# Performance work log

Measured on AMD Instinct MI355X. Metric: run time of the kernel, lower is better.

Reference implementation:

```python
import jax, jax.numpy as jnp
import numpy as np

B, S, D, H = 4, 2048, 1024, 16
HD = D // H  # head_dim = 64


def setup_inputs() -> dict:
    key = jax.random.key(0)
    ks = jax.random.split(key, 5)
    scale = 1.0 / np.sqrt(D)  # xavier-ish
    return {
        "query": jax.random.normal(ks[0], (B, S, D), dtype=jnp.float32),
        "Wq": jax.random.normal(ks[1], (D, D), dtype=jnp.float32) * scale,
        "bq": jnp.zeros((D,), dtype=jnp.float32),
        "Wk": jax.random.normal(ks[2], (D, D), dtype=jnp.float32) * scale,
        "bk": jnp.zeros((D,), dtype=jnp.float32),
        "Wv": jax.random.normal(ks[3], (D, D), dtype=jnp.float32) * scale,
        "bv": jnp.zeros((D,), dtype=jnp.float32),
        "Wo": jax.random.normal(ks[4], (D, D), dtype=jnp.float32) * scale,
        "bo": jnp.zeros((D,), dtype=jnp.float32),
    }


def reference(query, Wq, bq, Wk, bk, Wv, bv, Wo, bo):
    # Self-attention: key = value = query. Linear layers use y = x @ W^T + b (torch nn.Linear).
    q = query @ Wq.T + bq
    k = query @ Wk.T + bk
    v = query @ Wv.T + bv
    # [B, S, D] -> [B, H, S, HD]
    q = q.reshape(B, S, H, HD).transpose(0, 2, 1, 3)
    k = k.reshape(B, S, H, HD).transpose(0, 2, 1, 3)
    v = v.reshape(B, S, H, HD).transpose(0, 2, 1, 3)
    scores = jnp.einsum('bhqd,bhkd->bhqk', q, k) / jnp.sqrt(jnp.float32(HD))
    attn = jax.nn.softmax(scores, axis=-1)  # dropout=0 (eval)
    out = jnp.einsum('bhqk,bhkd->bhqd', attn, v)
    out = out.transpose(0, 2, 1, 3).reshape(B, S, D)
    out = out @ Wo.T + bo
    return out
```

## Files before the change

kernel.cpp:

```cpp
#include <hip/hip_runtime.h>
#include <cstdint>


#define B_ 4
#define S_ 2048
#define D_ 1024
#define H_ 16
#define HD_ 64
#define QKV_N 3072
#define QK_LD 2048
#define SCALE_Q 0.18033688011111772f

typedef __bf16 bf16x8 __attribute__((ext_vector_type(8)));
typedef __bf16 bf16x2 __attribute__((ext_vector_type(2)));
typedef float f32x4 __attribute__((ext_vector_type(4)));
typedef short short8 __attribute__((ext_vector_type(8)));

__device__ __forceinline__ unsigned short f2bf(float f) {
  unsigned int u = __builtin_bit_cast(unsigned int, f);
  u = (u + 0x7FFFu + ((u >> 16) & 1u)) >> 16;
  return (unsigned short)u;
}

__device__ __forceinline__ unsigned int pkbf(float a, float b) {
  bf16x2 v;
  v.x = (__bf16)a;
  v.y = (__bf16)b;
  return __builtin_bit_cast(unsigned int, v);
}

__device__ __forceinline__ void gload16(const void* g, void* l) {
  __builtin_amdgcn_global_load_lds(
      (const __attribute__((address_space(1))) void*)g,
      (__attribute__((address_space(3))) void*)l, 16, 0, 0);
}

__global__ __launch_bounds__(256) void cvt_bf16(const float* __restrict__ in,
                                                unsigned short* __restrict__ out, int n8) {
  int i = blockIdx.x * 256 + threadIdx.x;
  if (i >= n8) return;
  const float4* p = (const float4*)in + (size_t)i * 2;
  float4 a = p[0], b = p[1];
  unsigned short o[8] = {f2bf(a.x), f2bf(a.y), f2bf(a.z), f2bf(a.w),
                         f2bf(b.x), f2bf(b.y), f2bf(b.z), f2bf(b.w)};
  *(uint4*)(out + (size_t)i * 8) = *(const uint4*)o;
}

__global__ __launch_bounds__(256) void cvt_w4(const float* __restrict__ w0, const float* __restrict__ w1,
                                              const float* __restrict__ w2, const float* __restrict__ w3,
                                              unsigned short* __restrict__ dst) {
  int y = blockIdx.y;
  const float* src = (y == 0) ? w0 : (y == 1) ? w1 : (y == 2) ? w2 : w3;
  float s = (y == 0) ? SCALE_Q : 1.0f;
  int i = blockIdx.x * 256 + threadIdx.x;
  const float4* p = (const float4*)src + (size_t)i * 2;
  float4 a = p[0], b = p[1];
  unsigned short o[8] = {f2bf(a.x * s), f2bf(a.y * s), f2bf(a.z * s), f2bf(a.w * s),
                         f2bf(b.x * s), f2bf(b.y * s), f2bf(b.z * s), f2bf(b.w * s)};
  *(uint4*)(dst + (size_t)y * 1048576 + (size_t)i * 8) = *(const uint4*)o;
}

__global__ __launch_bounds__(256) void bias_cat(const float* __restrict__ bq, const float* __restrict__ bk,
                                                const float* __restrict__ bv, float* __restrict__ bcat) {
  int i = blockIdx.x * 256 + threadIdx.x;
  float v = (i < 1024) ? bq[i] * SCALE_Q : (i < 2048) ? bk[i - 1024] : bv[i - 2048];
  bcat[i] = v;
}

__device__ __forceinline__ void ld_afrag(const unsigned short* s, int rowbase, int quad,
                                         int sw, bf16x8 af[4][2]) {
#pragma unroll
  for (int mi2 = 0; mi2 < 4; ++mi2) {
    int row = rowbase + mi2 * 16;
#pragma unroll
    for (int kk = 0; kk < 2; ++kk)
      af[mi2][kk] = *(const bf16x8*)&s[row * 64 + ((((kk << 2) + quad) ^ sw) << 3)];
  }
}

__device__ __forceinline__ void ld_bfrag(const unsigned short* s, int rowbase, int quad,
                                         int sw, bf16x8 bf[2][2]) {
#pragma unroll
  for (int ni2 = 0; ni2 < 2; ++ni2) {
    int row = rowbase + ni2 * 16;
#pragma unroll
    for (int kk = 0; kk < 2; ++kk)
      bf[ni2][kk] = *(const bf16x8*)&s[row * 64 + ((((kk << 2) + quad) ^ sw) << 3)];
  }
}

#define SBAR() __builtin_amdgcn_sched_barrier(0)
#define BARRIER()                      \
  do {                                 \
    SBAR();                            \
    __builtin_amdgcn_s_barrier();      \
    SBAR();                            \
  } while (0)
#define WAITLGKM()                                      \
  do {                                                  \
    asm volatile("s_waitcnt lgkmcnt(0)" ::: "memory");  \
    SBAR();                                             \
  } while (0)

#define MM(qm, qn, BF)                                                                   \
  _Pragma("unroll") for (int mi2 = 0; mi2 < 4; ++mi2)                                    \
  _Pragma("unroll") for (int ni2 = 0; ni2 < 2; ++ni2)                                    \
  _Pragma("unroll") for (int kk = 0; kk < 2; ++kk)                                       \
      acc[(qm) * 4 + mi2][(qn) * 2 + ni2] = __builtin_amdgcn_mfma_f32_16x16x32_bf16(     \
          af[mi2][kk], BF[ni2][kk], acc[(qm) * 4 + mi2][(qn) * 2 + ni2], 0, 0, 0);

__global__ __launch_bounds__(512, 2) void gemm_qkv_256(
    const unsigned short* __restrict__ A, const unsigned short* __restrict__ W,
    const float* __restrict__ bias, unsigned short* __restrict__ qk,
    unsigned short* __restrict__ vt) {
  __shared__ __attribute__((aligned(16))) unsigned short sA[2][256 * 64];
  __shared__ __attribute__((aligned(16))) unsigned short sB[2][256 * 64];

  const int t = threadIdx.x;
  const int lane = t & 63;
  const int w = t >> 6;
  const int lm = lane & 15;
  const int quad = lane >> 4;
  const int sw = lm & 7;
  const int wm = (w >> 2) * 128;
  const int wn = (w & 3) * 64;

  const int bid = blockIdx.x;
  const int xcd = bid & 7, lin = bid >> 3;
  const int mt = xcd * 4 + (lin & 3);
  const int nt = lin >> 2;
  const int m0 = mt * 256, n0 = nt * 256;
  const int K = 1024;

  const int srow = t >> 3;
  const int scol = ((t & 7) ^ ((t >> 3) & 7)) << 3;
  const unsigned short* Ab = A + ((size_t)m0 + srow) * K + scol;
  const unsigned short* Wb = W + ((size_t)n0 + srow) * K + scol;

#define STG_A(bb, q, kt) gload16(Ab + (size_t)((q) * 64) * K + (kt), &sA[bb][(q) * 4096 + w * 512])
#define STG_B(bb, q, kt) gload16(Wb + (size_t)((q) * 64) * K + (kt), &sB[bb][(q) * 4096 + w * 512])

  STG_A(0, 0, 0); STG_A(0, 1, 0); STG_A(0, 2, 0); STG_A(0, 3, 0);
  STG_B(0, 0, 0); STG_B(0, 1, 0); STG_B(0, 2, 0); STG_B(0, 3, 0);
  STG_A(1, 0, 64); STG_A(1, 2, 64);
  STG_B(1, 0, 64); STG_B(1, 1, 64);
  STG_A(1, 1, 64); STG_A(1, 3, 64);
  asm volatile("s_waitcnt vmcnt(6)" ::: "memory");
  BARRIER();

  f32x4 acc[8][4] = {};
  bf16x8 af[4][2], bf0[2][2], bf1[2][2];

#define GROUP(c, kn1, kn2)                                                            \
  do {                                                                                \
    ld_afrag(sA[c], wm + lm, quad, sw, af);                                           \
    ld_bfrag(sB[c], wn + lm, quad, sw, bf0);                                          \
    STG_B(c ^ 1, 2, kn1);                                                             \
    STG_B(c ^ 1, 3, kn1);                                                             \
    BARRIER(); WAITLGKM();                                                            \
    __builtin_amdgcn_s_setprio(1); MM(0, 0, bf0); __builtin_amdgcn_s_setprio(0);      \
    BARRIER();                                                                        \
    ld_bfrag(sB[c], wn + 32 + lm, quad, sw, bf1);                                     \
    STG_A(c, 0, kn2);                                                                 \
    STG_A(c, 2, kn2);                                                                 \
    BARRIER(); WAITLGKM();                                                            \
    __builtin_amdgcn_s_setprio(1); MM(0, 1, bf1); __builtin_amdgcn_s_setprio(0);      \
    BARRIER();                                                                        \
    ld_afrag(sA[c], wm + 64 + lm, quad, sw, af);                                      \
    STG_B(c, 0, kn2);                                                                 \
    STG_B(c, 1, kn2);                                                                 \
    BARRIER(); WAITLGKM();                                                            \
    __builtin_amdgcn_s_setprio(1); MM(1, 0, bf0); __builtin_amdgcn_s_setprio(0);      \
    BARRIER();                                                                        \
    STG_A(c, 1, kn2);                                                                 \
    STG_A(c, 3, kn2);                                                                 \
    asm volatile("s_waitcnt vmcnt(6)" ::: "memory");                                  \
    BARRIER();                                                                        \
    __builtin_amdgcn_s_setprio(1); MM(1, 1, bf1); __builtin_amdgcn_s_setprio(0);      \
    BARRIER();                                                                        \
  } while (0)

  for (int kt = 0; kt < K; kt += 128) {
    const int kn1a = kt + 64;
    const int kn2a = (kt + 128 < K) ? kt + 128 : K - 64;
    const int kn1b = kn2a;
    const int kn2b = (kt + 192 < K) ? kt + 192 : K - 64;
    GROUP(0, kn1a, kn2a);
    GROUP(1, kn1b, kn2b);
  }

  asm volatile("s_waitcnt vmcnt(0)" ::: "memory");

#pragma unroll
  for (int mi = 0; mi < 8; ++mi) {
    const int rbase = m0 + wm + mi * 16 + quad * 4;
#pragma unroll
    for (int ni = 0; ni < 4; ++ni) {
      const int col = n0 + wn + ni * 16 + lm;
      const float bv = bias[col];
      float v0 = acc[mi][ni][0] + bv, v1 = acc[mi][ni][1] + bv;
      float v2 = acc[mi][ni][2] + bv, v3 = acc[mi][ni][3] + bv;
      if (n0 < 2048) {
        qk[(size_t)(rbase + 0) * QK_LD + col] = f2bf(v0);
        qk[(size_t)(rbase + 1) * QK_LD + col] = f2bf(v1);
        qk[(size_t)(rbase + 2) * QK_LD + col] = f2bf(v2);
        qk[(size_t)(rbase + 3) * QK_LD + col] = f2bf(v3);
      } else {
        int c = col - 2048;
        int bh = (m0 >> 11) * 16 + (c >> 6);
        int hd = c & 63;
        int sbase = rbase & 2047;
        uint2 pk = {pkbf(v0, v1), pkbf(v2, v3)};
        *(uint2*)(vt + (size_t)bh * (HD_ * S_) + (size_t)hd * S_ + sbase) = pk;
      }
    }
  }
}

__global__ __launch_bounds__(256) void gemm_bt(
    const unsigned short* __restrict__ A, const unsigned short* __restrict__ W,
    const float* __restrict__ bias, void* __restrict__ Cout,
    unsigned short* __restrict__ vt, int M, int N, int K, int mode) {
  __shared__ __attribute__((aligned(16))) unsigned short sA[128 * 32];
  __shared__ __attribute__((aligned(16))) unsigned short sB[128 * 32];
  const int t = threadIdx.x;
  const int lane = t & 63;
  const int w = t >> 6;
  const int lm = lane & 15;
  const int quad = lane >> 4;
  const int m0 = blockIdx.x * 128;
  const int n0 = blockIdx.y * 128;
  const int wm = (w & 1) * 64;
  const int wn = (w >> 1) * 64;

  const int off0 = t * 8, off1 = t * 8 + 2048;
  const int ar0 = off0 >> 5, ac0 = (((off0 >> 3) & 3) ^ ((ar0 >> 1) & 3)) * 8;
  const int ar1 = off1 >> 5, ac1 = (((off1 >> 3) & 3) ^ ((ar1 >> 1) & 3)) * 8;
  const unsigned short* Ag0 = A + (size_t)(m0 + ar0) * K + ac0;
  const unsigned short* Ag1 = A + (size_t)(m0 + ar1) * K + ac1;
  const unsigned short* Wg0 = W + (size_t)(n0 + ar0) * K + ac0;
  const unsigned short* Wg1 = W + (size_t)(n0 + ar1) * K + ac1;
  unsigned short* sA0 = &sA[w * 512];
  unsigned short* sA1 = &sA[2048 + w * 512];
  unsigned short* sB0 = &sB[w * 512];
  unsigned short* sB1 = &sB[2048 + w * 512];

  f32x4 acc[4][4] = {};

  for (int kt = 0; kt < K; kt += 32) {
    gload16(Ag0 + kt, sA0);
    gload16(Ag1 + kt, sA1);
    gload16(Wg0 + kt, sB0);
    gload16(Wg1 + kt, sB1);
    __syncthreads();
    bf16x8 af[4], bf[4];
#pragma unroll
    for (int mi = 0; mi < 4; ++mi) {
      int row = wm + mi * 16 + lm;
      af[mi] = *(const bf16x8*)&sA[row * 32 + ((quad ^ ((row >> 1) & 3)) << 3)];
    }
#pragma unroll
    for (int ni = 0; ni < 4; ++ni) {
      int row = wn + ni * 16 + lm;
      bf[ni] = *(const bf16x8*)&sB[row * 32 + ((quad ^ ((row >> 1) & 3)) << 3)];
    }
#pragma unroll
    for (int mi = 0; mi < 4; ++mi)
#pragma unroll
      for (int ni = 0; ni < 4; ++ni)
        acc[mi][ni] = __builtin_amdgcn_mfma_f32_16x16x32_bf16(af[mi], bf[ni], acc[mi][ni], 0, 0, 0);
    __syncthreads();
  }

#pragma unroll
  for (int mi = 0; mi < 4; ++mi)
#pragma unroll
    for (int ni = 0; ni < 4; ++ni) {
      int col = n0 + wn + ni * 16 + lm;
      float bv = bias[col];
      float v0 = acc[mi][ni][0] + bv, v1 = acc[mi][ni][1] + bv;
      float v2 = acc[mi][ni][2] + bv, v3 = acc[mi][ni][3] + bv;
      int rbase = m0 + wm + mi * 16 + quad * 4;
      if (mode == 0) {
        float* op = (float*)Cout;
        op[(size_t)(rbase + 0) * N + col] = v0;
        op[(size_t)(rbase + 1) * N + col] = v1;
        op[(size_t)(rbase + 2) * N + col] = v2;
        op[(size_t)(rbase + 3) * N + col] = v3;
      } else if (col < 2048) {
        unsigned short* op = (unsigned short*)Cout;
        op[(size_t)(rbase + 0) * QK_LD + col] = f2bf(v0);
        op[(size_t)(rbase + 1) * QK_LD + col] = f2bf(v1);
        op[(size_t)(rbase + 2) * QK_LD + col] = f2bf(v2);
        op[(size_t)(rbase + 3) * QK_LD + col] = f2bf(v3);
      } else {
        int c = col - 2048;
        int bh = (m0 >> 11) * 16 + (c >> 6);
        int hd = c & 63;
        int sbase = (rbase & 2047);
        uint2 pk = {pkbf(v0, v1), pkbf(v2, v3)};
        *(uint2*)(vt + (size_t)bh * (HD_ * S_) + (size_t)hd * S_ + sbase) = pk;
      }
    }
}

__global__ __launch_bounds__(512, 4) void attn_kernel(
    const unsigned short* __restrict__ qk, const unsigned short* __restrict__ vt,
    unsigned short* __restrict__ ab) {
  __shared__ __attribute__((aligned(16))) unsigned short sK[2][64 * 64];
  __shared__ __attribute__((aligned(16))) unsigned short sV[2][64 * 64];
  __shared__ __attribute__((aligned(16))) unsigned short sP[8][32 * 64];

  const int t = threadIdx.x;
  const int lane = t & 63;
  const int w = t >> 6;
  const int lm = lane & 15;
  const int quad = lane >> 4;
  const int bh = blockIdx.x & 63;
  const int b = bh >> 4, h = bh & 15;
  const int q0 = (blockIdx.x >> 6) * 256;

  const unsigned short* qg = qk + (size_t)b * S_ * QK_LD + h * HD_;
  const unsigned short* kg = qg + 1024;
  const unsigned short* vg = vt + (size_t)bh * HD_ * S_;

  const int r0 = t >> 3;
  const int c0 = ((t & 7) ^ (r0 & 7)) * 8;

  gload16(kg + (size_t)r0 * QK_LD + c0, &sK[0][w * 512]);
  gload16(vg + (size_t)r0 * S_ + c0, &sV[0][w * 512]);

  bf16x8 qf[2][2];
#pragma unroll
  for (int mi = 0; mi < 2; ++mi) {
    int row = q0 + w * 32 + mi * 16 + lm;
#pragma unroll
    for (int kc = 0; kc < 2; ++kc)
      qf[mi][kc] = *(const bf16x8*)(qg + (size_t)row * QK_LD + kc * 32 + quad * 8);
  }
  __syncthreads();

  unsigned short* sPw = sP[w];
  const bf16x8 ones = __builtin_bit_cast(bf16x8, (short8)(short)0x3F80);
  f32x4 o[2][4] = {};
  f32x4 Lacc[2] = {};

  for (int n0 = 0; n0 < S_; n0 += 64) {
    const int cur = (n0 >> 6) & 1, nxt = cur ^ 1;
    if (n0 + 64 < S_) {
      gload16(kg + (size_t)(n0 + 64 + r0) * QK_LD + c0, &sK[nxt][w * 512]);
      gload16(vg + (size_t)r0 * S_ + (n0 + 64) + c0, &sV[nxt][w * 512]);
    }

    f32x4 s[2][4] = {};
#pragma unroll
    for (int kc = 0; kc < 2; ++kc)
#pragma unroll
      for (int nb = 0; nb < 4; ++nb) {
        int row = nb * 16 + lm;
        bf16x8 kf = *(const bf16x8*)&sK[cur][row * 64 + (((kc * 4 + quad) ^ (row & 7)) << 3)];
#pragma unroll
        for (int mi = 0; mi < 2; ++mi)
          s[mi][nb] = __builtin_amdgcn_mfma_f32_16x16x32_bf16(kf, qf[mi][kc], s[mi][nb], 0, 0, 0);
      }

#pragma unroll
    for (int mi = 0; mi < 2; ++mi) {
      int prow = mi * 16 + lm;
      char* rowp = (char*)sPw + prow * 128;
#pragma unroll
      for (int nb = 0; nb < 4; ++nb) {
        const f32x4& sv = s[mi][nb];
        uint2 pk = {pkbf(__builtin_amdgcn_exp2f(sv[0]), __builtin_amdgcn_exp2f(sv[1])),
                    pkbf(__builtin_amdgcn_exp2f(sv[2]), __builtin_amdgcn_exp2f(sv[3]))};
        int c16 = (nb * 2 + (quad >> 1)) ^ (prow & 7);
        *(uint2*)(rowp + (c16 << 4) + ((quad & 1) << 3)) = pk;
      }
    }

#pragma unroll
    for (int kc = 0; kc < 2; ++kc) {
      bf16x8 pf[2];
#pragma unroll
      for (int mi = 0; mi < 2; ++mi) {
        int prow = mi * 16 + lm;
        pf[mi] = *(const bf16x8*)&sPw[prow * 64 + (((kc * 4 + quad) ^ (prow & 7)) << 3)];
        Lacc[mi] = __builtin_amdgcn_mfma_f32_16x16x32_bf16(pf[mi], ones, Lacc[mi], 0, 0, 0);
      }
#pragma unroll
      for (int nf = 0; nf < 4; ++nf) {
        int row = nf * 16 + lm;
        bf16x8 vf = *(const bf16x8*)&sV[cur][row * 64 + (((kc * 4 + quad) ^ (row & 7)) << 3)];
#pragma unroll
        for (int mi = 0; mi < 2; ++mi)
          o[mi][nf] = __builtin_amdgcn_mfma_f32_16x16x32_bf16(pf[mi], vf, o[mi][nf], 0, 0, 0);
      }
    }
    __syncthreads();
  }

#pragma unroll
  for (int mi = 0; mi < 2; ++mi)
#pragma unroll
    for (int r = 0; r < 4; ++r) {
      float rinv = 1.0f / Lacc[mi][r];
      int row = q0 + w * 32 + mi * 16 + quad * 4 + r;
#pragma unroll
      for (int nf = 0; nf < 4; ++nf) {
        int col = h * HD_ + nf * 16 + lm;
        ab[(size_t)(b * S_ + row) * D_ + col] = f2bf(o[mi][nf][r] * rinv);
      }
    }
}

extern "C" void kernel_launch(void* const* d_in, const int* in_sizes, int n_in,
                              void* d_out, int out_size, void* d_ws, size_t ws_size,
                              hipStream_t stream) {
  const float* x = (const float*)d_in[0];
  const float* Wq = (const float*)d_in[1];
  const float* bq = (const float*)d_in[2];
  const float* Wk = (const float*)d_in[3];
  const float* bk = (const float*)d_in[4];
  const float* Wv = (const float*)d_in[5];
  const float* bv = (const float*)d_in[6];
  const float* Wo = (const float*)d_in[7];
  const float* bo = (const float*)d_in[8];
  float* out = (float*)d_out;

  const size_t E = (size_t)B_ * S_ * D_;
  const size_t WE = (size_t)D_ * D_;
  unsigned short* xb = (unsigned short*)d_ws;
  unsigned short* wcat = xb + E;
  unsigned short* wob = wcat + 3 * WE;
  float* bcat = (float*)(wcat + 4 * WE);
  unsigned short* qkb = (unsigned short*)(bcat + 4096);
  unsigned short* vtb = qkb + (size_t)B_ * S_ * QK_LD;
  unsigned short* abuf = xb;

  cvt_bf16<<<dim3((unsigned)(E / 8 / 256)), 256, 0, stream>>>(x, xb, (int)(E / 8));
  cvt_w4<<<dim3(512, 4), 256, 0, stream>>>(Wq, Wk, Wv, Wo, wcat);
  bias_cat<<<dim3(12), 256, 0, stream>>>(bq, bk, bv, bcat);

  gemm_qkv_256<<<dim3(384), 512, 0, stream>>>(xb, wcat, bcat, qkb, vtb);
  attn_kernel<<<dim3(512), 512, 0, stream>>>(qkb, vtb, abuf);
  gemm_bt<<<dim3((B_ * S_) / 128, D_ / 128), 256, 0, stream>>>(
      abuf, wob, bo, out, nullptr, B_ * S_, D_, D_, 0);
}
```

Baseline: 283.5 us.

## Simplify QKV GEMM pipeline to full-tile double buffering and fuse conversion kernels

```diff
diff --git a/kernel.cpp b/kernel.cpp
--- a/kernel.cpp
+++ b/kernel.cpp
@@ -35,36 +35,37 @@
       (__attribute__((address_space(3))) void*)l, 16, 0, 0);
 }
 
-__global__ __launch_bounds__(256) void cvt_bf16(const float* __restrict__ in,
-                                                unsigned short* __restrict__ out, int n8) {
-  int i = blockIdx.x * 256 + threadIdx.x;
-  if (i >= n8) return;
-  const float4* p = (const float4*)in + (size_t)i * 2;
-  float4 a = p[0], b = p[1];
-  unsigned short o[8] = {f2bf(a.x), f2bf(a.y), f2bf(a.z), f2bf(a.w),
-                         f2bf(b.x), f2bf(b.y), f2bf(b.z), f2bf(b.w)};
-  *(uint4*)(out + (size_t)i * 8) = *(const uint4*)o;
-}
-
-__global__ __launch_bounds__(256) void cvt_w4(const float* __restrict__ w0, const float* __restrict__ w1,
-                                              const float* __restrict__ w2, const float* __restrict__ w3,
-                                              unsigned short* __restrict__ dst) {
-  int y = blockIdx.y;
-  const float* src = (y == 0) ? w0 : (y == 1) ? w1 : (y == 2) ? w2 : w3;
-  float s = (y == 0) ? SCALE_Q : 1.0f;
-  int i = blockIdx.x * 256 + threadIdx.x;
-  const float4* p = (const float4*)src + (size_t)i * 2;
-  float4 a = p[0], b = p[1];
-  unsigned short o[8] = {f2bf(a.x * s), f2bf(a.y * s), f2bf(a.z * s), f2bf(a.w * s),
-                         f2bf(b.x * s), f2bf(b.y * s), f2bf(b.z * s), f2bf(b.w * s)};
-  *(uint4*)(dst + (size_t)y * 1048576 + (size_t)i * 8) = *(const uint4*)o;
-}
-
-__global__ __launch_bounds__(256) void bias_cat(const float* __restrict__ bq, const float* __restrict__ bk,
-                                                const float* __restrict__ bv, float* __restrict__ bcat) {
-  int i = blockIdx.x * 256 + threadIdx.x;
-  float v = (i < 1024) ? bq[i] * SCALE_Q : (i < 2048) ? bk[i - 1024] : bv[i - 2048];
-  bcat[i] = v;
+__global__ __launch_bounds__(256) void cvt_all(
+    const float* __restrict__ x, const float* __restrict__ w0, const float* __restrict__ w1,
+    const float* __restrict__ w2, const float* __restrict__ w3,
+    const float* __restrict__ bq, const float* __restrict__ bk, const float* __restrict__ bv,
+    unsigned short* __restrict__ xb, unsigned short* __restrict__ wcat,
+    float* __restrict__ bcat) {
+  const int blk = blockIdx.x;
+  const int t = threadIdx.x;
+  if (blk < 4096) {
+    size_t i = (size_t)blk * 256 + t;
+    const float4* p = (const float4*)x + i * 2;
+    float4 a = p[0], b = p[1];
+    unsigned short o[8] = {f2bf(a.x), f2bf(a.y), f2bf(a.z), f2bf(a.w),
+                           f2bf(b.x), f2bf(b.y), f2bf(b.z), f2bf(b.w)};
+    *(uint4*)(xb + i * 8) = *(const uint4*)o;
+  } else if (blk < 6144) {
+    int y = (blk - 4096) >> 9;
+    const float* src = (y == 0) ? w0 : (y == 1) ? w1 : (y == 2) ? w2 : w3;
+    float s = (y == 0) ? SCALE_Q : 1.0f;
+    size_t i = (size_t)((blk - 4096) & 511) * 256 + t;
+    const float4* p = (const float4*)src + i * 2;
+    float4 a = p[0], b = p[1];
+    unsigned short o[8] = {f2bf(a.x * s), f2bf(a.y * s), f2bf(a.z * s), f2bf(a.w * s),
+                           f2bf(b.x * s), f2bf(b.y * s), f2bf(b.z * s), f2bf(b.w * s)};
+    *(uint4*)(wcat + (size_t)y * 1048576 + i * 8) = *(const uint4*)o;
+  } else {
+    for (int i = t; i < 3072; i += 256) {
+      float v = (i < 1024) ? bq[i] * SCALE_Q : (i < 2048) ? bk[i - 1024] : bv[i - 2048];
+      bcat[i] = v;
+    }
+  }
 }
 
 __device__ __forceinline__ void ld_afrag(const unsigned short* s, int rowbase, int quad,
@@ -78,14 +79,14 @@
   }
 }
 
-__device__ __forceinline__ void ld_bfrag(const unsigned short* s, int rowbase, int quad,
-                                         int sw, bf16x8 bf[2][2]) {
-#pragma unroll
-  for (int ni2 = 0; ni2 < 2; ++ni2) {
-    int row = rowbase + ni2 * 16;
+__device__ __forceinline__ void ld_bfrag4(const unsigned short* s, int rowbase, int quad,
+                                          int sw, bf16x8 bf[4][2]) {
+#pragma unroll
+  for (int ni = 0; ni < 4; ++ni) {
+    int row = rowbase + ni * 16;
 #pragma unroll
     for (int kk = 0; kk < 2; ++kk)
-      bf[ni2][kk] = *(const bf16x8*)&s[row * 64 + ((((kk << 2) + quad) ^ sw) << 3)];
+      bf[ni][kk] = *(const bf16x8*)&s[row * 64 + ((((kk << 2) + quad) ^ sw) << 3)];
   }
 }
 
@@ -102,12 +103,12 @@
     SBAR();                                             \
   } while (0)
 
-#define MM(qm, qn, BF)                                                                   \
+#define MM32(qm)                                                                         \
   _Pragma("unroll") for (int mi2 = 0; mi2 < 4; ++mi2)                                    \
-  _Pragma("unroll") for (int ni2 = 0; ni2 < 2; ++ni2)                                    \
+  _Pragma("unroll") for (int ni = 0; ni < 4; ++ni)                                       \
   _Pragma("unroll") for (int kk = 0; kk < 2; ++kk)                                       \
-      acc[(qm) * 4 + mi2][(qn) * 2 + ni2] = __builtin_amdgcn_mfma_f32_16x16x32_bf16(     \
-          af[mi2][kk], BF[ni2][kk], acc[(qm) * 4 + mi2][(qn) * 2 + ni2], 0, 0, 0);
+      acc[(qm) * 4 + mi2][ni] = __builtin_amdgcn_mfma_f32_16x16x32_bf16(                 \
+          af[mi2][kk], bf[ni][kk], acc[(qm) * 4 + mi2][ni], 0, 0, 0);
 
 __global__ __launch_bounds__(512, 2) void gemm_qkv_256(
     const unsigned short* __restrict__ A, const unsigned short* __restrict__ W,
@@ -139,54 +140,31 @@
 
 #define STG_A(bb, q, kt) gload16(Ab + (size_t)((q) * 64) * K + (kt), &sA[bb][(q) * 4096 + w * 512])
 #define STG_B(bb, q, kt) gload16(Wb + (size_t)((q) * 64) * K + (kt), &sB[bb][(q) * 4096 + w * 512])
-
-  STG_A(0, 0, 0); STG_A(0, 1, 0); STG_A(0, 2, 0); STG_A(0, 3, 0);
-  STG_B(0, 0, 0); STG_B(0, 1, 0); STG_B(0, 2, 0); STG_B(0, 3, 0);
-  STG_A(1, 0, 64); STG_A(1, 2, 64);
-  STG_B(1, 0, 64); STG_B(1, 1, 64);
-  STG_A(1, 1, 64); STG_A(1, 3, 64);
-  asm volatile("s_waitcnt vmcnt(6)" ::: "memory");
-  BARRIER();
+#define STG_TILE(bb, kt)                                              \
+  do {                                                                \
+    STG_A(bb, 0, kt); STG_A(bb, 1, kt); STG_A(bb, 2, kt); STG_A(bb, 3, kt); \
+    STG_B(bb, 0, kt); STG_B(bb, 1, kt); STG_B(bb, 2, kt); STG_B(bb, 3, kt); \
+  } while (0)
+
+  STG_TILE(0, 0);
 
   f32x4 acc[8][4] = {};
-  bf16x8 af[4][2], bf0[2][2], bf1[2][2];
-
-#define GROUP(c, kn1, kn2)                                                            \
-  do {                                                                                \
-    ld_afrag(sA[c], wm + lm, quad, sw, af);                                           \
-    ld_bfrag(sB[c], wn + lm, quad, sw, bf0);                                          \
-    STG_B(c ^ 1, 2, kn1);                                                             \
-    STG_B(c ^ 1, 3, kn1);                                                             \
-    BARRIER(); WAITLGKM();                                                            \
-    __builtin_amdgcn_s_setprio(1); MM(0, 0, bf0); __builtin_amdgcn_s_setprio(0);      \
-    BARRIER();                                                                        \
-    ld_bfrag(sB[c], wn + 32 + lm, quad, sw, bf1);                                     \
-    STG_A(c, 0, kn2);                                                                 \
-    STG_A(c, 2, kn2);                                                                 \
-    BARRIER(); WAITLGKM();                                                            \
-    __builtin_amdgcn_s_setprio(1); MM(0, 1, bf1); __builtin_amdgcn_s_setprio(0);      \
-    BARRIER();                                                                        \
-    ld_afrag(sA[c], wm + 64 + lm, quad, sw, af);                                      \
-    STG_B(c, 0, kn2);                                                                 \
-    STG_B(c, 1, kn2);                                                                 \
-    BARRIER(); WAITLGKM();                                                            \
-    __builtin_amdgcn_s_setprio(1); MM(1, 0, bf0); __builtin_amdgcn_s_setprio(0);      \
-    BARRIER();                                                                        \
-    STG_A(c, 1, kn2);                                                                 \
-    STG_A(c, 3, kn2);                                                                 \
-    asm volatile("s_waitcnt vmcnt(6)" ::: "memory");                                  \
-    BARRIER();                                                                        \
-    __builtin_amdgcn_s_setprio(1); MM(1, 1, bf1); __builtin_amdgcn_s_setprio(0);      \
-    BARRIER();                                                                        \
-  } while (0)
-
-  for (int kt = 0; kt < K; kt += 128) {
-    const int kn1a = kt + 64;
-    const int kn2a = (kt + 128 < K) ? kt + 128 : K - 64;
-    const int kn1b = kn2a;
-    const int kn2b = (kt + 192 < K) ? kt + 192 : K - 64;
-    GROUP(0, kn1a, kn2a);
-    GROUP(1, kn1b, kn2b);
+  bf16x8 af[4][2], bf[4][2];
+
+  for (int tt = 0; tt < 16; ++tt) {
+    const int c = tt & 1;
+    const int kn = (tt + 1 < 16 ? tt + 1 : 15) * 64;
+    STG_TILE(c ^ 1, kn);
+    asm volatile("s_waitcnt vmcnt(8)" ::: "memory");
+    BARRIER();
+    ld_afrag(sA[c], wm + lm, quad, sw, af);
+    ld_bfrag4(sB[c], wn + lm, quad, sw, bf);
+    WAITLGKM();
+    __builtin_amdgcn_s_setprio(1); MM32(0); __builtin_amdgcn_s_setprio(0);
+    ld_afrag(sA[c], wm + 64 + lm, quad, sw, af);
+    WAITLGKM();
+    __builtin_amdgcn_s_setprio(1); MM32(1); __builtin_amdgcn_s_setprio(0);
+    BARRIER();
   }
 
   asm volatile("s_waitcnt vmcnt(0)" ::: "memory");
@@ -206,9 +184,9 @@
         qk[(size_t)(rbase + 2) * QK_LD + col] = f2bf(v2);
         qk[(size_t)(rbase + 3) * QK_LD + col] = f2bf(v3);
       } else {
-        int c = col - 2048;
-        int bh = (m0 >> 11) * 16 + (c >> 6);
-        int hd = c & 63;
+        int c2 = col - 2048;
+        int bh = (m0 >> 11) * 16 + (c2 >> 6);
+        int hd = c2 & 63;
         int sbase = rbase & 2047;
         uint2 pk = {pkbf(v0, v1), pkbf(v2, v3)};
         *(uint2*)(vt + (size_t)bh * (HD_ * S_) + (size_t)hd * S_ + sbase) = pk;
@@ -437,9 +415,7 @@
   unsigned short* vtb = qkb + (size_t)B_ * S_ * QK_LD;
   unsigned short* abuf = xb;
 
-  cvt_bf16<<<dim3((unsigned)(E / 8 / 256)), 256, 0, stream>>>(x, xb, (int)(E / 8));
-  cvt_w4<<<dim3(512, 4), 256, 0, stream>>>(Wq, Wk, Wv, Wo, wcat);
-  bias_cat<<<dim3(12), 256, 0, stream>>>(bq, bk, bv, bcat);
+  cvt_all<<<dim3(6145), 256, 0, stream>>>(x, Wq, Wk, Wv, Wo, bq, bk, bv, xb, wcat, bcat);
 
   gemm_qkv_256<<<dim3(384), 512, 0, stream>>>(xb, wcat, bcat, qkb, vtb);
   attn_kernel<<<dim3(512), 512, 0, stream>>>(qkb, vtb, abuf);
```

New measurement: 276.5 us. 2.5% less time.

## Replace output projection GEMM with pipelined 256x128 tile kernel and merge conversion kernels

Applied to the files above, without the earlier changes.

```diff
diff --git a/kernel.cpp b/kernel.cpp
--- a/kernel.cpp
+++ b/kernel.cpp
@@ -35,36 +35,37 @@
       (__attribute__((address_space(3))) void*)l, 16, 0, 0);
 }
 
-__global__ __launch_bounds__(256) void cvt_bf16(const float* __restrict__ in,
-                                                unsigned short* __restrict__ out, int n8) {
-  int i = blockIdx.x * 256 + threadIdx.x;
-  if (i >= n8) return;
-  const float4* p = (const float4*)in + (size_t)i * 2;
-  float4 a = p[0], b = p[1];
-  unsigned short o[8] = {f2bf(a.x), f2bf(a.y), f2bf(a.z), f2bf(a.w),
-                         f2bf(b.x), f2bf(b.y), f2bf(b.z), f2bf(b.w)};
-  *(uint4*)(out + (size_t)i * 8) = *(const uint4*)o;
-}
-
-__global__ __launch_bounds__(256) void cvt_w4(const float* __restrict__ w0, const float* __restrict__ w1,
-                                              const float* __restrict__ w2, const float* __restrict__ w3,
-                                              unsigned short* __restrict__ dst) {
-  int y = blockIdx.y;
-  const float* src = (y == 0) ? w0 : (y == 1) ? w1 : (y == 2) ? w2 : w3;
-  float s = (y == 0) ? SCALE_Q : 1.0f;
-  int i = blockIdx.x * 256 + threadIdx.x;
-  const float4* p = (const float4*)src + (size_t)i * 2;
-  float4 a = p[0], b = p[1];
-  unsigned short o[8] = {f2bf(a.x * s), f2bf(a.y * s), f2bf(a.z * s), f2bf(a.w * s),
-                         f2bf(b.x * s), f2bf(b.y * s), f2bf(b.z * s), f2bf(b.w * s)};
-  *(uint4*)(dst + (size_t)y * 1048576 + (size_t)i * 8) = *(const uint4*)o;
-}
-
-__global__ __launch_bounds__(256) void bias_cat(const float* __restrict__ bq, const float* __restrict__ bk,
-                                                const float* __restrict__ bv, float* __restrict__ bcat) {
-  int i = blockIdx.x * 256 + threadIdx.x;
-  float v = (i < 1024) ? bq[i] * SCALE_Q : (i < 2048) ? bk[i - 1024] : bv[i - 2048];
-  bcat[i] = v;
+__global__ __launch_bounds__(256) void cvt_all(
+    const float* __restrict__ x, const float* __restrict__ w0, const float* __restrict__ w1,
+    const float* __restrict__ w2, const float* __restrict__ w3,
+    const float* __restrict__ bq, const float* __restrict__ bk, const float* __restrict__ bv,
+    unsigned short* __restrict__ xb, unsigned short* __restrict__ wcat,
+    float* __restrict__ bcat) {
+  const int blk = blockIdx.x;
+  const int t = threadIdx.x;
+  if (blk < 4096) {
+    size_t i = (size_t)blk * 256 + t;
+    const float4* p = (const float4*)x + i * 2;
+    float4 a = p[0], b = p[1];
+    unsigned short o[8] = {f2bf(a.x), f2bf(a.y), f2bf(a.z), f2bf(a.w),
+                           f2bf(b.x), f2bf(b.y), f2bf(b.z), f2bf(b.w)};
+    *(uint4*)(xb + i * 8) = *(const uint4*)o;
+  } else if (blk < 6144) {
+    int y = (blk - 4096) >> 9;
+    const float* src = (y == 0) ? w0 : (y == 1) ? w1 : (y == 2) ? w2 : w3;
+    float s = (y == 0) ? SCALE_Q : 1.0f;
+    size_t i = (size_t)((blk - 4096) & 511) * 256 + t;
+    const float4* p = (const float4*)src + i * 2;
+    float4 a = p[0], b = p[1];
+    unsigned short o[8] = {f2bf(a.x * s), f2bf(a.y * s), f2bf(a.z * s), f2bf(a.w * s),
+                           f2bf(b.x * s), f2bf(b.y * s), f2bf(b.z * s), f2bf(b.w * s)};
+    *(uint4*)(wcat + (size_t)y * 1048576 + i * 8) = *(const uint4*)o;
+  } else {
+    for (int i = t; i < 3072; i += 256) {
+      float v = (i < 1024) ? bq[i] * SCALE_Q : (i < 2048) ? bk[i - 1024] : bv[i - 2048];
+      bcat[i] = v;
+    }
+  }
 }
 
 __device__ __forceinline__ void ld_afrag(const unsigned short* s, int rowbase, int quad,
@@ -87,6 +88,13 @@
     for (int kk = 0; kk < 2; ++kk)
       bf[ni2][kk] = *(const bf16x8*)&s[row * 64 + ((((kk << 2) + quad) ^ sw) << 3)];
   }
+}
+
+__device__ __forceinline__ void ld_b2(const unsigned short* s, int row, int quad,
+                                      int sw, bf16x8 bf[2]) {
+#pragma unroll
+  for (int kk = 0; kk < 2; ++kk)
+    bf[kk] = *(const bf16x8*)&s[row * 64 + ((((kk << 2) + quad) ^ sw) << 3)];
 }
 
 #define SBAR() __builtin_amdgcn_sched_barrier(0)
@@ -206,9 +214,9 @@
         qk[(size_t)(rbase + 2) * QK_LD + col] = f2bf(v2);
         qk[(size_t)(rbase + 3) * QK_LD + col] = f2bf(v3);
       } else {
-        int c = col - 2048;
-        int bh = (m0 >> 11) * 16 + (c >> 6);
-        int hd = c & 63;
+        int c2 = col - 2048;
+        int bh = (m0 >> 11) * 16 + (c2 >> 6);
+        int hd = c2 & 63;
         int sbase = rbase & 2047;
         uint2 pk = {pkbf(v0, v1), pkbf(v2, v3)};
         *(uint2*)(vt + (size_t)bh * (HD_ * S_) + (size_t)hd * S_ + sbase) = pk;
@@ -217,91 +225,96 @@
   }
 }
 
-__global__ __launch_bounds__(256) void gemm_bt(
+#define MM8(qm, ni, BF)                                                                  \
+  _Pragma("unroll") for (int mi2 = 0; mi2 < 4; ++mi2)                                    \
+  _Pragma("unroll") for (int kk = 0; kk < 2; ++kk)                                       \
+      acc[(qm) * 4 + mi2][ni] = __builtin_amdgcn_mfma_f32_16x16x32_bf16(                 \
+          af[mi2][kk], BF[kk], acc[(qm) * 4 + mi2][ni], 0, 0, 0);
+
+__global__ __launch_bounds__(512, 2) void gemm_out_256(
     const unsigned short* __restrict__ A, const unsigned short* __restrict__ W,
-    const float* __restrict__ bias, void* __restrict__ Cout,
-    unsigned short* __restrict__ vt, int M, int N, int K, int mode) {
-  __shared__ __attribute__((aligned(16))) unsigned short sA[128 * 32];
-  __shared__ __attribute__((aligned(16))) unsigned short sB[128 * 32];
+    const float* __restrict__ bias, float* __restrict__ out) {
+  __shared__ __attribute__((aligned(16))) unsigned short sA[2][256 * 64];
+  __shared__ __attribute__((aligned(16))) unsigned short sB[2][128 * 64];
+
   const int t = threadIdx.x;
   const int lane = t & 63;
   const int w = t >> 6;
   const int lm = lane & 15;
   const int quad = lane >> 4;
-  const int m0 = blockIdx.x * 128;
-  const int n0 = blockIdx.y * 128;
-  const int wm = (w & 1) * 64;
-  const int wn = (w >> 1) * 64;
-
-  const int off0 = t * 8, off1 = t * 8 + 2048;
-  const int ar0 = off0 >> 5, ac0 = (((off0 >> 3) & 3) ^ ((ar0 >> 1) & 3)) * 8;
-  const int ar1 = off1 >> 5, ac1 = (((off1 >> 3) & 3) ^ ((ar1 >> 1) & 3)) * 8;
-  const unsigned short* Ag0 = A + (size_t)(m0 + ar0) * K + ac0;
-  const unsigned short* Ag1 = A + (size_t)(m0 + ar1) * K + ac1;
-  const unsigned short* Wg0 = W + (size_t)(n0 + ar0) * K + ac0;
-  const unsigned short* Wg1 = W + (size_t)(n0 + ar1) * K + ac1;
-  unsigned short* sA0 = &sA[w * 512];
-  unsigned short* sA1 = &sA[2048 + w * 512];
-  unsigned short* sB0 = &sB[w * 512];
-  unsigned short* sB1 = &sB[2048 + w * 512];
-
-  f32x4 acc[4][4] = {};
-
-  for (int kt = 0; kt < K; kt += 32) {
-    gload16(Ag0 + kt, sA0);
-    gload16(Ag1 + kt, sA1);
-    gload16(Wg0 + kt, sB0);
-    gload16(Wg1 + kt, sB1);
-    __syncthreads();
-    bf16x8 af[4], bf[4];
-#pragma unroll
-    for (int mi = 0; mi < 4; ++mi) {
-      int row = wm + mi * 16 + lm;
-      af[mi] = *(const bf16x8*)&sA[row * 32 + ((quad ^ ((row >> 1) & 3)) << 3)];
-    }
-#pragma unroll
-    for (int ni = 0; ni < 4; ++ni) {
-      int row = wn + ni * 16 + lm;
-      bf[ni] = *(const bf16x8*)&sB[row * 32 + ((quad ^ ((row >> 1) & 3)) << 3)];
-    }
-#pragma unroll
-    for (int mi = 0; mi < 4; ++mi)
-#pragma unroll
-      for (int ni = 0; ni < 4; ++ni)
-        acc[mi][ni] = __builtin_amdgcn_mfma_f32_16x16x32_bf16(af[mi], bf[ni], acc[mi][ni], 0, 0, 0);
-    __syncthreads();
-  }
-
-#pragma unroll
-  for (int mi = 0; mi < 4; ++mi)
-#pragma unroll
-    for (int ni = 0; ni < 4; ++ni) {
-      int col = n0 + wn + ni * 16 + lm;
-      float bv = bias[col];
-      float v0 = acc[mi][ni][0] + bv, v1 = acc[mi][ni][1] + bv;
-      float v2 = acc[mi][ni][2] + bv, v3 = acc[mi][ni][3] + bv;
-      int rbase = m0 + wm + mi * 16 + quad * 4;
-      if (mode == 0) {
-        float* op = (float*)Cout;
-        op[(size_t)(rbase + 0) * N + col] = v0;
-        op[(size_t)(rbase + 1) * N + col] = v1;
-        op[(size_t)(rbase + 2) * N + col] = v2;
-        op[(size_t)(rbase + 3) * N + col] = v3;
-      } else if (col < 2048) {
-        unsigned short* op = (unsigned short*)Cout;
-        op[(size_t)(rbase + 0) * QK_LD + col] = f2bf(v0);
-        op[(size_t)(rbase + 1) * QK_LD + col] = f2bf(v1);
-        op[(size_t)(rbase + 2) * QK_LD + col] = f2bf(v2);
-        op[(size_t)(rbase + 3) * QK_LD + col] = f2bf(v3);
-      } else {
-        int c = col - 2048;
-        int bh = (m0 >> 11) * 16 + (c >> 6);
-        int hd = c & 63;
-        int sbase = (rbase & 2047);
-        uint2 pk = {pkbf(v0, v1), pkbf(v2, v3)};
-        *(uint2*)(vt + (size_t)bh * (HD_ * S_) + (size_t)hd * S_ + sbase) = pk;
-      }
-    }
+  const int sw = lm & 7;
+  const int wm = (w >> 2) * 128;
+  const int wn = (w & 3) * 32;
+
+  const int bid = blockIdx.x;
+  const int xcd = bid & 7, lin = bid >> 3;
+  const int mt = xcd * 4 + (lin & 3);
+  const int nt = lin >> 2;
+  const int m0 = mt * 256, n0 = nt * 128;
+  const int K = 1024;
+
+  const int srow = t >> 3;
+  const int scol = ((t & 7) ^ ((t >> 3) & 7)) << 3;
+  const unsigned short* Ab = A + ((size_t)m0 + srow) * K + scol;
+  const unsigned short* Wb = W + ((size_t)n0 + srow) * K + scol;
+
+#define OSTG_A(bb, q, kt) gload16(Ab + (size_t)((q) * 64) * K + (kt), &sA[bb][(q) * 4096 + w * 512])
+#define OSTG_B(bb, q, kt) gload16(Wb + (size_t)((q) * 64) * K + (kt), &sB[bb][(q) * 4096 + w * 512])
+
+  OSTG_A(0, 0, 0); OSTG_A(0, 1, 0); OSTG_A(0, 2, 0); OSTG_A(0, 3, 0);
+  OSTG_B(0, 0, 0); OSTG_B(0, 1, 0);
+  OSTG_A(1, 0, 64); OSTG_A(1, 2, 64);
+  OSTG_A(1, 1, 64); OSTG_A(1, 3, 64);
+  asm volatile("s_waitcnt vmcnt(4)" ::: "memory");
+  BARRIER();
+
+  f32x4 acc[8][2] = {};
+  bf16x8 af[4][2], bf0[2], bf1[2];
+
+  for (int tt = 0; tt < 16; ++tt) {
+    const int c = tt & 1;
+    const int knB = (tt + 1 < 16 ? tt + 1 : 15) * 64;
+    const int knA = (tt + 2 < 16 ? tt + 2 : 15) * 64;
+    ld_afrag(sA[c], wm + lm, quad, sw, af);
+    ld_b2(sB[c], wn + lm, quad, sw, bf0);
+    OSTG_B(c ^ 1, 0, knB);
+    OSTG_B(c ^ 1, 1, knB);
+    BARRIER(); WAITLGKM();
+    __builtin_amdgcn_s_setprio(1); MM8(0, 0, bf0); __builtin_amdgcn_s_setprio(0);
+    BARRIER();
+    ld_b2(sB[c], wn + 16 + lm, quad, sw, bf1);
+    OSTG_A(c, 0, knA);
+    OSTG_A(c, 2, knA);
+    BARRIER(); WAITLGKM();
+    __builtin_amdgcn_s_setprio(1); MM8(0, 1, bf1); __builtin_amdgcn_s_setprio(0);
+    BARRIER();
+    ld_afrag(sA[c], wm + 64 + lm, quad, sw, af);
+    BARRIER(); WAITLGKM();
+    __builtin_amdgcn_s_setprio(1); MM8(1, 0, bf0); __builtin_amdgcn_s_setprio(0);
+    BARRIER();
+    OSTG_A(c, 1, knA);
+    OSTG_A(c, 3, knA);
+    asm volatile("s_waitcnt vmcnt(4)" ::: "memory");
+    BARRIER();
+    __builtin_amdgcn_s_setprio(1); MM8(1, 1, bf1); __builtin_amdgcn_s_setprio(0);
+    BARRIER();
+  }
+
+  asm volatile("s_waitcnt vmcnt(0)" ::: "memory");
+
+#pragma unroll
+  for (int mi = 0; mi < 8; ++mi) {
+    const int rbase = m0 + wm + mi * 16 + quad * 4;
+#pragma unroll
+    for (int ni = 0; ni < 2; ++ni) {
+      const int col = n0 + wn + ni * 16 + lm;
+      const float bv = bias[col];
+      out[(size_t)(rbase + 0) * D_ + col] = acc[mi][ni][0] + bv;
+      out[(size_t)(rbase + 1) * D_ + col] = acc[mi][ni][1] + bv;
+      out[(size_t)(rbase + 2) * D_ + col] = acc[mi][ni][2] + bv;
+      out[(size_t)(rbase + 3) * D_ + col] = acc[mi][ni][3] + bv;
+    }
+  }
 }
 
 __global__ __launch_bounds__(512, 4) void attn_kernel(
@@ -437,12 +450,9 @@
   unsigned short* vtb = qkb + (size_t)B_ * S_ * QK_LD;
   unsigned short* abuf = xb;
 
-  cvt_bf16<<<dim3((unsigned)(E / 8 / 256)), 256, 0, stream>>>(x, xb, (int)(E / 8));
-  cvt_w4<<<dim3(512, 4), 256, 0, stream>>>(Wq, Wk, Wv, Wo, wcat);
-  bias_cat<<<dim3(12), 256, 0, stream>>>(bq, bk, bv, bcat);
+  cvt_all<<<dim3(6145), 256, 0, stream>>>(x, Wq, Wk, Wv, Wo, bq, bk, bv, xb, wcat, bcat);
 
   gemm_qkv_256<<<dim3(384), 512, 0, stream>>>(xb, wcat, bcat, qkb, vtb);
   attn_kernel<<<dim3(512), 512, 0, stream>>>(qkb, vtb, abuf);
-  gemm_bt<<<dim3((B_ * S_) / 128, D_ / 128), 256, 0, stream>>>(
-      abuf, wob, bo, out, nullptr, B_ * S_, D_, D_, 0);
-}
+  gemm_out_256<<<dim3(256), 512, 0, stream>>>(abuf, wob, bo, out);
+}
```

Measured after the change: 276.1 us. 1.03x faster.
